# Performance work log

Hardware: AMD Instinct MI355X
Metric: run time of the kernel (lower is better)

## Reference

```python
import jax, jax.numpy as jnp
import numpy as np

B, T, E, H = 2048, 128, 192, 192
SCALE = E ** (-0.5)  # original scales by embed_size**-0.5, not head_size


def setup_inputs() -> dict:
    key = jax.random.key(0)
    k1, k2, k3, k4 = jax.random.split(key, 4)
    x = jax.random.normal(k1, (B, T, E), dtype=jnp.float32)
    # torch Linear weights: [out_features, in_features]
    Wq = jax.random.normal(k2, (H, E), dtype=jnp.float32) * (E ** -0.5)
    Wk = jax.random.normal(k3, (H, E), dtype=jnp.float32) * (E ** -0.5)
    Wv = jax.random.normal(k4, (H, E), dtype=jnp.float32) * (E ** -0.5)
    return {"x": x, "Wq": Wq, "Wk": Wk, "Wv": Wv}


def reference(x, Wq, Wk, Wv):
    # projections: y = x @ W.T (torch Linear, no bias)
    q = jnp.einsum("bte,he->bth", x, Wq)
    k = jnp.einsum("bte,he->bth", x, Wk)
    v = jnp.einsum("bte,he->bth", x, Wv)
    wei = jnp.einsum("bqh,bkh->bqk", q, k) * SCALE  # [B,T,T]
    causal = jnp.tril(jnp.ones((T, T), dtype=bool))
    wei = jnp.where(causal, wei, -jnp.inf)
    wei = jax.nn.softmax(wei, axis=-1)
    # dropout omitted: eval-mode (deterministic) reference
    return jnp.einsum("bqk,bkh->bqh", wei, v)
```

## Files before the change

kernel.cpp:

```cpp
#include <hip/hip_runtime.h>
#include <hip/hip_bf16.h>

#define TT 128
#define EE 192
#define HH 192
#define SCALE_F 0.07216878364870322f
#define LOG2E_F 1.4426950408889634f

typedef float f32x4 __attribute__((ext_vector_type(4)));
typedef short short8 __attribute__((ext_vector_type(8)));
typedef short short4v __attribute__((ext_vector_type(4)));

__device__ inline unsigned short f2bf(float x) {
  union { float f; unsigned u; } v; v.f = x;
  unsigned r = v.u + 0x7FFFu + ((v.u >> 16) & 1u);
  return (unsigned short)(r >> 16);
}
__device__ inline unsigned pack2bf(float a, float b) {
  __hip_bfloat162 h = __float22bfloat162_rn(float2{a, b});
  union { __hip_bfloat162 h2; unsigned u; } c; c.h2 = h;
  return c.u;
}

__global__ void pack_wv(const float* __restrict__ Wv, short* __restrict__ out) {
  int f = blockIdx.x * 4 + (threadIdx.x >> 6);
  int lane = threadIdx.x & 63, lg = lane >> 4, lr = lane & 15;
  int tile = f / 6, es = f % 6;
  const float* p = Wv + (16 * tile + lr) * EE + 32 * es + 8 * lg;
  float4 a = *(const float4*)p;
  float4 b = *(const float4*)(p + 4);
  short8 h;
  h[0] = (short)f2bf(a.x); h[1] = (short)f2bf(a.y);
  h[2] = (short)f2bf(a.z); h[3] = (short)f2bf(a.w);
  h[4] = (short)f2bf(b.x); h[5] = (short)f2bf(b.y);
  h[6] = (short)f2bf(b.z); h[7] = (short)f2bf(b.w);
  *(short8*)(out + ((size_t)f * 64 + lane) * 8) = h;
}

__global__ __launch_bounds__(256)
void make_mt(const float* __restrict__ Wq, const float* __restrict__ Wk,
             short* __restrict__ out) {
  __shared__ float red[4][64][8];
  const int f = blockIdx.x;
  const int tid = threadIdx.x;
  const int w = tid >> 6, lane = tid & 63, lg = lane >> 4, lr = lane & 15;
  const int tile = f / 6, es = f % 6;
  const int kcol = 16 * tile + lr;
  const int e1b = 32 * es + 8 * lg;

  float acc[8];
#pragma unroll
  for (int j = 0; j < 8; ++j) acc[j] = 0.f;
#pragma unroll 4
  for (int h = 48 * w; h < 48 * w + 48; ++h) {
    float kv = Wk[h * EE + kcol];
    const float* qp = Wq + h * EE + e1b;
    float4 q0 = *(const float4*)qp, q1 = *(const float4*)(qp + 4);
    acc[0] += q0.x * kv; acc[1] += q0.y * kv;
    acc[2] += q0.z * kv; acc[3] += q0.w * kv;
    acc[4] += q1.x * kv; acc[5] += q1.y * kv;
    acc[6] += q1.z * kv; acc[7] += q1.w * kv;
  }
#pragma unroll
  for (int j = 0; j < 8; ++j) red[w][lane][j] = acc[j];
  __syncthreads();
  if (w == 0) {
    union { unsigned d[4]; short8 s; } h;
#pragma unroll
    for (int i = 0; i < 4; ++i) {
      float a = red[0][lane][2*i]   + red[1][lane][2*i]   + red[2][lane][2*i]   + red[3][lane][2*i];
      float b = red[0][lane][2*i+1] + red[1][lane][2*i+1] + red[2][lane][2*i+1] + red[3][lane][2*i+1];
      h.d[i] = pack2bf(a, b);
    }
    *(short8*)((char*)out + (size_t)f * 1024 + lane * 16) = h.s;
  }
}

__device__ __forceinline__ void proj_v(const char* smem, const short* wfv,
                                       int nt, char* vgb, int mtoff,
                                       int lg, int lr) {
  const f32x4 zero = {0.f, 0.f, 0.f, 0.f};
  const int lane = lg * 16 + lr;
  short8 wg[6];
#pragma unroll
  for (int i = 0; i < 6; ++i)
    wg[i] = *(const short8*)((const char*)wfv + ((size_t)(nt * 6 + i) * 64 + lane) * 16);
#pragma unroll
  for (int mt = 0; mt < 4; ++mt) {
    f32x4 a0 = zero;
#pragma unroll
    for (int es = 0; es < 6; ++es) {
      short8 xf = *(const short8*)(smem + (mt * 6 + es) * 1024 + lane * 16);
      a0 = __builtin_amdgcn_mfma_f32_16x16x32_bf16(xf, wg[es], a0, 0, 0, 0);
    }
    int mtg = mtoff + mt;
    union { unsigned d[2]; short4v v; } pu;
    pu.d[0] = pack2bf(a0[0], a0[1]);
    pu.d[1] = pack2bf(a0[2], a0[3]);
    *(short4v*)(vgb + (size_t)((mtg >> 1) * 12 + nt) * 1024 +
                ((2 * (mtg & 1) + (lg >> 1)) * 16 + lr) * 16 + (lg & 1) * 8) = pu.v;
  }
}

__global__ __launch_bounds__(512)
void v_gemm(const float* __restrict__ x, const short* __restrict__ wfv,
            char* __restrict__ kvws) {
  __shared__ char smem[24576];
  const int bh = blockIdx.x, b = bh >> 1, half = bh & 1;
  const int tid = threadIdx.x;
  const int w = tid >> 6, lane = tid & 63, lg = lane >> 4, lr = lane & 15;
  const float4* xb4 = (const float4*)(x + (size_t)b * (TT * EE) + (size_t)half * 64 * EE);
  char* kvb = kvws + (size_t)b * 98304;

#pragma unroll
  for (int i = 0; i < 6; ++i) {
    int fi = tid + 512 * i;
    int t = fi / 48, c4 = fi % 48;
    float4 f = xb4[fi];
    union { unsigned d[2]; short4v s; } h4;
    h4.d[0] = pack2bf(f.x, f.y);
    h4.d[1] = pack2bf(f.z, f.w);
    int loff = ((t >> 4) * 6 + (c4 >> 3)) * 1024 +
               ((((c4 & 7) >> 1) << 4) + (t & 15)) * 16 + ((c4 & 1) << 3);
    *(short4v*)(smem + loff) = h4.s;
  }
  __syncthreads();

#pragma unroll
  for (int i = 0; i < 3; ++i) {
    int off = (w * 3 + i) * 1024 + lane * 16;
    short8 v = *(const short8*)(smem + off);
    *(short8*)(kvb + (size_t)half * 24576 + off) = v;
  }

  const int mtoff = half * 4;
  char* vgb = kvb + 49152;
  proj_v(smem, wfv, w, vgb, mtoff, lg, lr);
  if (w < 4) proj_v(smem, wfv, 8 + w, vgb, mtoff, lg, lr);
}

__global__ __launch_bounds__(512)
void attn_y(const short* __restrict__ wfy, char* __restrict__ kv) {
  __shared__ char smem[49152];
  const int b = blockIdx.x;
  const int tid = threadIdx.x;
  const int qt = tid >> 6, lane = tid & 63, lg = lane >> 4, lr = lane & 15;
  const char* xfb = kv + (size_t)b * 98304;
  const char* vb  = xfb + 49152;
  const char* wyc = (const char*)wfy;
  const f32x4 zero = {0.f, 0.f, 0.f, 0.f};

  short8 xfr[6];
#pragma unroll
  for (int i = 0; i < 6; ++i)
    xfr[i] = *(const short8*)(xfb + (qt * 6 + i) * 1024 + lane * 16);

  unsigned wqp[12][2];
#pragma unroll
  for (int h = 0; h < 2; ++h) {
    if (h == 1) __syncthreads();
#pragma unroll
    for (int i = 0; i < 5; ++i) {
      int idx = tid + 512 * i;
      if (idx < 2304)
        *(short8*)(smem + idx * 16) =
            *(const short8*)(wyc + (size_t)h * 36864 + (size_t)idx * 16);
    }
    __syncthreads();
#pragma unroll
    for (int ht2 = 0; ht2 < 6; ++ht2) {
      f32x4 a = zero;
#pragma unroll
      for (int es = 0; es < 6; ++es) {
        short8 wg = *(const short8*)(smem + (ht2 * 6 + es) * 1024 + lane * 16);
        a = __builtin_amdgcn_mfma_f32_16x16x32_bf16(wg, xfr[es], a, 0, 0, 0);
      }
      wqp[6 * h + ht2][0] = pack2bf(a[0], a[1]);
      wqp[6 * h + ht2][1] = pack2bf(a[2], a[3]);
    }
  }

  short8 vreg[6];
#pragma unroll
  for (int i = 0; i < 6; ++i)
    vreg[i] = *(const short8*)(vb + (qt * 6 + i) * 1024 + lane * 16);

  short8 qb[6];
#pragma unroll
  for (int ha = 0; ha < 6; ++ha) {
    union { unsigned d[4]; short8 v; } au;
#pragma unroll
    for (int i = 0; i < 4; ++i) {
      int sl = ((2 * (lg & 1) + (i >> 1)) << 4) | lr;
      unsigned v0 = (unsigned)__shfl((int)wqp[2 * ha][i & 1], sl);
      unsigned v1 = (unsigned)__shfl((int)wqp[2 * ha + 1][i & 1], sl);
      au.d[i] = (lg >> 1) ? v1 : v0;
    }
    qb[ha] = au.v;
  }

  __syncthreads();
#pragma unroll
  for (int i = 0; i < 6; ++i)
    *(short8*)(smem + (qt * 6 + i) * 1024 + lane * 16) = xfr[i];
  __syncthreads();

  short8 pa[4];
  {
    f32x4 sa[8];
#pragma unroll
    for (int kt = 0; kt < 8; ++kt) sa[kt] = zero;
#pragma unroll
    for (int kt = 0; kt < 8; ++kt) {
      if (kt <= qt) {
#pragma unroll
        for (int ha = 0; ha < 6; ++ha) {
          short8 ka = *(const short8*)(smem + (kt * 6 + ha) * 1024 + lane * 16);
          sa[kt] = __builtin_amdgcn_mfma_f32_16x16x32_bf16(ka, qb[ha], sa[kt], 0, 0, 0);
        }
      }
    }

    const float CSC = SCALE_F * LOG2E_F;
    float m = -INFINITY;
#pragma unroll
    for (int kt = 0; kt < 8; ++kt)
      if (kt <= qt) {
#pragma unroll
        for (int r = 0; r < 4; ++r) {
          float v = sa[kt][r] * CSC;
          if (kt == qt && 4 * lg + r > lr) v = -INFINITY;
          sa[kt][r] = v;
          m = fmaxf(m, v);
        }
      }
    m = fmaxf(m, __shfl_xor(m, 16));
    m = fmaxf(m, __shfl_xor(m, 32));
    float sum = 0.f;
#pragma unroll
    for (int kt = 0; kt < 8; ++kt)
      if (kt <= qt) {
#pragma unroll
        for (int r = 0; r < 4; ++r) {
          float p = exp2f(sa[kt][r] - m);
          sa[kt][r] = p;
          sum += p;
        }
      }
    sum += __shfl_xor(sum, 16);
    sum += __shfl_xor(sum, 32);
    const float rinv = 1.0f / sum;

    unsigned pw[8][2];
#pragma unroll
    for (int kt = 0; kt < 8; ++kt) { pw[kt][0] = 0u; pw[kt][1] = 0u; }
#pragma unroll
    for (int kt = 0; kt < 8; ++kt)
      if (kt <= qt) {
        pw[kt][0] = pack2bf(sa[kt][0] * rinv, sa[kt][1] * rinv);
        pw[kt][1] = pack2bf(sa[kt][2] * rinv, sa[kt][3] * rinv);
      }

#pragma unroll
    for (int tp = 0; tp < 4; ++tp) {
      union { unsigned d[4]; short8 v; } au;
#pragma unroll
      for (int i = 0; i < 4; ++i) {
        int sl = ((2 * (lg & 1) + (i >> 1)) << 4) | lr;
        unsigned lo = (unsigned)__shfl((int)pw[2 * tp][i & 1], sl);
        unsigned hi = (unsigned)__shfl((int)pw[2 * tp + 1][i & 1], sl);
        au.d[i] = (lg >> 1) ? hi : lo;
      }
      pa[tp] = au.v;
    }
  }
  __syncthreads();

#pragma unroll
  for (int i = 0; i < 6; ++i)
    *(short8*)(smem + (qt * 6 + i) * 1024 + lane * 16) = vreg[i];
  __syncthreads();

  float* ob = (float*)(kv + (size_t)b * 98304);
#pragma unroll
  for (int half = 0; half < 2; ++half) {
    f32x4 o6[6];
#pragma unroll
    for (int n = 0; n < 6; ++n) o6[n] = zero;
#pragma unroll
    for (int tp = 0; tp < 4; ++tp) {
      if (tp <= (qt >> 1)) {
#pragma unroll
        for (int n = 0; n < 6; ++n) {
          int ht = half * 6 + n;
          short8 va = *(const short8*)(smem + (tp * 12 + ht) * 1024 + lane * 16);
          o6[n] = __builtin_amdgcn_mfma_f32_16x16x32_bf16(va, pa[tp], o6[n], 0, 0, 0);
        }
      }
    }
#pragma unroll
    for (int n = 0; n < 6; ++n)
      *(f32x4*)(ob + (16 * qt + lr) * HH + 16 * (half * 6 + n) + 4 * lg) = o6[n];
  }
}

extern "C" void kernel_launch(void* const* d_in, const int* in_sizes, int n_in,
                              void* d_out, int out_size, void* d_ws, size_t ws_size,
                              hipStream_t stream) {
  const float* x  = (const float*)d_in[0];
  const float* Wq = (const float*)d_in[1];
  const float* Wk = (const float*)d_in[2];
  const float* Wv = (const float*)d_in[3];
  int Bn = in_sizes[0] / (TT * EE);

  short* wfy = (short*)d_ws;
  short* wfv = wfy + 36864;

  hipLaunchKernelGGL(pack_wv, dim3(18), dim3(256), 0, stream, Wv, wfv);
  hipLaunchKernelGGL(make_mt, dim3(72), dim3(256), 0, stream, Wq, Wk, wfy);
  hipLaunchKernelGGL(v_gemm, dim3(2 * Bn), dim3(512), 0, stream,
                     x, wfv, (char*)d_out);
  hipLaunchKernelGGL(attn_y, dim3(Bn), dim3(512), 0, stream,
                     wfy, (char*)d_out);
}
```

Baseline: 206.6 us.

## Stage x and full Wqk into separate LDS buffers in attn_y, cut barriers

attn_y now uses 120KB of dynamic shared memory split into two regions: the bf16 x tile goes to A and the whole 73KB projection matrix goes to B in one cooperative load. This removes the two-phase weight reload, the later copy of x back into LDS, and several __syncthreads. V is then staged into B once the Q-projection is done. The larger LDS footprint limits occupancy to one block per CU, which may reduce latency hiding.

After: 194.2 us. 1.06x faster.

```diff
diff --git a/kernel.cpp b/kernel.cpp
--- a/kernel.cpp
+++ b/kernel.cpp
@@ -141,7 +141,9 @@
 
 __global__ __launch_bounds__(512)
 void attn_y(const short* __restrict__ wfy, char* __restrict__ kv) {
-  __shared__ char smem[49152];
+  extern __shared__ char smem[];
+  char* A = smem;
+  char* B = smem + 49152;
   const int b = blockIdx.x;
   const int tid = threadIdx.x;
   const int qt = tid >> 6, lane = tid & 63, lg = lane >> 4, lr = lane & 15;
@@ -150,40 +152,35 @@
   const char* wyc = (const char*)wfy;
   const f32x4 zero = {0.f, 0.f, 0.f, 0.f};
 
+#pragma unroll
+  for (int i = 0; i < 6; ++i) {
+    int off = (tid + 512 * i) * 16;
+    *(short8*)(A + off) = *(const short8*)(xfb + off);
+  }
+#pragma unroll
+  for (int i = 0; i < 9; ++i) {
+    int off = (tid + 512 * i) * 16;
+    *(short8*)(B + off) = *(const short8*)(wyc + off);
+  }
+  __syncthreads();
+
   short8 xfr[6];
 #pragma unroll
   for (int i = 0; i < 6; ++i)
-    xfr[i] = *(const short8*)(xfb + (qt * 6 + i) * 1024 + lane * 16);
+    xfr[i] = *(const short8*)(A + (qt * 6 + i) * 1024 + lane * 16);
 
   unsigned wqp[12][2];
 #pragma unroll
-  for (int h = 0; h < 2; ++h) {
-    if (h == 1) __syncthreads();
-#pragma unroll
-    for (int i = 0; i < 5; ++i) {
-      int idx = tid + 512 * i;
-      if (idx < 2304)
-        *(short8*)(smem + idx * 16) =
-            *(const short8*)(wyc + (size_t)h * 36864 + (size_t)idx * 16);
-    }
-    __syncthreads();
-#pragma unroll
-    for (int ht2 = 0; ht2 < 6; ++ht2) {
-      f32x4 a = zero;
-#pragma unroll
-      for (int es = 0; es < 6; ++es) {
-        short8 wg = *(const short8*)(smem + (ht2 * 6 + es) * 1024 + lane * 16);
-        a = __builtin_amdgcn_mfma_f32_16x16x32_bf16(wg, xfr[es], a, 0, 0, 0);
-      }
-      wqp[6 * h + ht2][0] = pack2bf(a[0], a[1]);
-      wqp[6 * h + ht2][1] = pack2bf(a[2], a[3]);
-    }
-  }
-
-  short8 vreg[6];
-#pragma unroll
-  for (int i = 0; i < 6; ++i)
-    vreg[i] = *(const short8*)(vb + (qt * 6 + i) * 1024 + lane * 16);
+  for (int ht = 0; ht < 12; ++ht) {
+    f32x4 a = zero;
+#pragma unroll
+    for (int es = 0; es < 6; ++es) {
+      short8 wg = *(const short8*)(B + (ht * 6 + es) * 1024 + lane * 16);
+      a = __builtin_amdgcn_mfma_f32_16x16x32_bf16(wg, xfr[es], a, 0, 0, 0);
+    }
+    wqp[ht][0] = pack2bf(a[0], a[1]);
+    wqp[ht][1] = pack2bf(a[2], a[3]);
+  }
 
   short8 qb[6];
 #pragma unroll
@@ -198,12 +195,12 @@
     }
     qb[ha] = au.v;
   }
-
-  __syncthreads();
+  __syncthreads();
+
+  short8 vreg[6];
 #pragma unroll
   for (int i = 0; i < 6; ++i)
-    *(short8*)(smem + (qt * 6 + i) * 1024 + lane * 16) = xfr[i];
-  __syncthreads();
+    vreg[i] = *(const short8*)(vb + (qt * 6 + i) * 1024 + lane * 16);
 
   short8 pa[4];
   {
@@ -215,7 +212,7 @@
       if (kt <= qt) {
 #pragma unroll
         for (int ha = 0; ha < 6; ++ha) {
-          short8 ka = *(const short8*)(smem + (kt * 6 + ha) * 1024 + lane * 16);
+          short8 ka = *(const short8*)(A + (kt * 6 + ha) * 1024 + lane * 16);
           sa[kt] = __builtin_amdgcn_mfma_f32_16x16x32_bf16(ka, qb[ha], sa[kt], 0, 0, 0);
         }
       }
@@ -274,11 +271,10 @@
       pa[tp] = au.v;
     }
   }
-  __syncthreads();
 
 #pragma unroll
   for (int i = 0; i < 6; ++i)
-    *(short8*)(smem + (qt * 6 + i) * 1024 + lane * 16) = vreg[i];
+    *(short8*)(B + (qt * 6 + i) * 1024 + lane * 16) = vreg[i];
   __syncthreads();
 
   float* ob = (float*)(kv + (size_t)b * 98304);
@@ -293,7 +289,7 @@
 #pragma unroll
         for (int n = 0; n < 6; ++n) {
           int ht = half * 6 + n;
-          short8 va = *(const short8*)(smem + (tp * 12 + ht) * 1024 + lane * 16);
+          short8 va = *(const short8*)(B + (tp * 12 + ht) * 1024 + lane * 16);
           o6[n] = __builtin_amdgcn_mfma_f32_16x16x32_bf16(va, pa[tp], o6[n], 0, 0, 0);
         }
       }
@@ -320,6 +316,6 @@
   hipLaunchKernelGGL(make_mt, dim3(72), dim3(256), 0, stream, Wq, Wk, wfy);
   hipLaunchKernelGGL(v_gemm, dim3(2 * Bn), dim3(512), 0, stream,
                      x, wfv, (char*)d_out);
-  hipLaunchKernelGGL(attn_y, dim3(Bn), dim3(512), 0, stream,
+  hipLaunchKernelGGL(attn_y, dim3(Bn), dim3(512), 122880, stream,
                      wfy, (char*)d_out);
 }
```
